# Kernel tuning notes

Hardware: AMD Instinct MI355X
Metric: run time of the kernel (lower is better)

## Reference

```python
import jax, jax.numpy as jnp
import numpy as np

B, N, K = 4, 4096, 16   # batch of graphs, nodes, kernel_size (label width)
C, T = 8, 3             # out_channels, convoTimes


def setup_inputs() -> dict:
    key = jax.random.key(0)
    k1, k2, k3 = jax.random.split(key, 3)
    labelsList = jax.random.normal(k1, (B, N, K), dtype=jnp.float32)
    # adjacency-like structure; WLC only tests >= 1, values in {0,1}
    ligand_structure = jax.random.randint(k2, (B, N, N), 0, 2, dtype=jnp.int32)
    # nn.ParameterDict of torch.rand(convoTimes, kernel_size) per channel -> [C, T, K]
    kernels = jax.random.uniform(k3, (C, T, K), dtype=jnp.float32)
    return {"labelsList": labelsList, "ligand_structure": ligand_structure, "kernels": kernels}


def reference(labelsList, ligand_structure, kernels):
    # mask[b,n,s] = 1 if ligand_structure[b][n][s] >= 1 (thresholded adjacency)
    mask = (ligand_structure >= 1).astype(labelsList.dtype)  # [B,N,N]
    # newLabelsList = labelsList.repeat(out_channels,1,1) -> [B,C,N,K]
    X0 = jnp.broadcast_to(labelsList[:, None], (B, C, N, K))
    # Each convo step reads a snapshot (cal_list) taken before the step, so:
    #   X_{t+1}[c] = X_t[c] + (mask @ X_t[c]) * kernels[c, t]
    def step(X, kt):  # kt: [C,K] = kernels[:, t, :]
        agg = jnp.einsum('bns,bcsk->bcnk', mask, X)  # masked sparse-dense matmul
        return X + agg * kt[None, :, None, :], None

    Xf, _ = jax.lax.scan(step, X0, jnp.swapaxes(kernels, 0, 1))  # scan over T steps
    return Xf  # [B,C,N,K]
```

## Files before the change

kernel.cpp:

```cpp
#include <hip/hip_runtime.h>


#define BB 4
#define NN 4096
#define KK 16
#define CC 8
#define TT 3
#define WPR (NN / 64)
#define YSWZ (KK * NN)

typedef unsigned long long u64;
typedef unsigned int u32;
typedef unsigned short u16;
typedef __attribute__((ext_vector_type(8))) short s16x8;
typedef __attribute__((ext_vector_type(4))) float f32x4v;

__device__ __forceinline__ u32 bf16_rne(float f) {
    u32 u = __float_as_uint(f);
    return (u + 0x7FFFu + ((u >> 16) & 1u)) >> 16;
}
__device__ __forceinline__ float bf16_f32(u32 h) {
    return __uint_as_float(h << 16);
}
__device__ __forceinline__ long ypos(int f, int s) {
    return ((long)(s >> 8) << 12) + (s & 3) * 1024 + ((s >> 7) & 1) * 512 +
           f * 32 + ((s >> 5) & 3) * 8 + ((s >> 2) & 7);
}

__device__ __forceinline__ s16x8 expand8(u32 byt) {
    u32 n0 = byt & 0xFu, n1 = (byt >> 4) & 0xFu;
    u32 t0 = (n0 * 0x204081u) & 0x01010101u;
    u32 t1 = (n1 * 0x204081u) & 0x01010101u;
    u32 m0 = (t0 << 7) - t0;
    u32 m1 = (t1 << 7) - t1;
    union { u32 w[4]; s16x8 v; } u;
    u.w[0] = __builtin_amdgcn_perm(0u, m0, 0x0C010C00u) << 7;
    u.w[1] = __builtin_amdgcn_perm(0u, m0, 0x0C030C02u) << 7;
    u.w[2] = __builtin_amdgcn_perm(0u, m1, 0x0C010C00u) << 7;
    u.w[3] = __builtin_amdgcn_perm(0u, m1, 0x0C030C02u) << 7;
    return u.v;
}

__global__ __launch_bounds__(256)
void prep_kernel(const float* __restrict__ labels, u16* __restrict__ ysw0) {
    int gid = blockIdx.x * 256 + threadIdx.x;
    int s4 = (gid & (NN / 4 - 1)) * 4;
    int f  = (gid >> 10) & (KK - 1);
    int b  = gid >> 14;
    long base = (long)b * YSWZ + ypos(f, s4);
    const float* lp = labels + ((long)b * NN + s4) * KK + f;
#pragma unroll
    for (int j = 0; j < 4; ++j)
        ysw0[base + j * 1024] = (u16)bf16_rne(lp[j * KK]);
}

__global__ __launch_bounds__(256, 4)
void spmm1_k(const int* __restrict__ lig, u64* __restrict__ bits,
             const u16* __restrict__ yin, u16* __restrict__ yout)
{
    __shared__ float red[3][4][64];
    __shared__ u64 bl[64][16];
    const int bid = blockIdx.x;
    const int rt  = bid & (NN / 16 - 1);
    const int b   = bid >> 8;
    const int tid = threadIdx.x;
    const int lane = tid & 63, ss = tid >> 6;
    const int n16 = lane & 15, g = lane >> 4;
    const int row0 = rt * 16;

    const u16* yb = yin + (long)b * YSWZ + (ss * 16) * 1024 + n16 * 32 + g * 8;
    s16x8 p0[4], p1[4];
#pragma unroll
    for (int i = 0; i < 4; ++i) {
        p0[i] = *(const s16x8*)(yb + i * 1024);
        p1[i] = *(const s16x8*)(yb + i * 1024 + 512);
    }

    {
        const int* lrow = lig + ((long)b * NN + row0) * NN;
        auto laddr = [&](int i) {
            int row = (ss * 4) + (i >> 4), w4 = i & 15;
            return (const int4*)(lrow + (long)row * NN + w4 * 256 + lane * 4);
        };
        int4 v[4];
#pragma unroll
        for (int i = 0; i < 4; ++i) v[i] = *laddr(i);
#pragma unroll 4
        for (int i = 0; i < 64; ++i) {
            const int slot = i & 3;
            int4 cur = v[slot];
            if (i + 4 < 64) v[slot] = *laddr(i + 4);
            u64 m0 = __ballot(cur.x >= 1);
            u64 m1 = __ballot(cur.y >= 1);
            u64 m2 = __ballot(cur.z >= 1);
            u64 m3 = __ballot(cur.w >= 1);
            if (lane == 0) {
                int row = (ss * 4) + (i >> 4), wq = (i & 15) * 4;
                bl[wq + 0][row] = m0; bl[wq + 1][row] = m1;
                bl[wq + 2][row] = m2; bl[wq + 3][row] = m3;
            }
        }
        __syncthreads();
        uint4* dst = (uint4*)(bits + (long)(b * (NN / 16) + rt) * 1024);
        const uint4* src = (const uint4*)&bl[0][0];
        dst[tid]       = src[tid];
        dst[tid + 256] = src[tid + 256];
    }

    u64 wcs[16];
#pragma unroll
    for (int wi = 0; wi < 16; ++wi) wcs[wi] = bl[ss * 16 + wi][n16];

    f32x4v accA = {0.f, 0.f, 0.f, 0.f}, accB = {0.f, 0.f, 0.f, 0.f};
#pragma unroll
    for (int wi = 0; wi < 16; ++wi) {
        const int slot = wi & 3;
        s16x8 b0 = p0[slot], b1 = p1[slot];
        if (wi + 4 < 16) {
            p0[slot] = *(const s16x8*)(yb + (wi + 4) * 1024);
            p1[slot] = *(const s16x8*)(yb + (wi + 4) * 1024 + 512);
        }
        u64 h = wcs[wi] >> (g * 8);
        accA = __builtin_amdgcn_mfma_f32_16x16x32_bf16(expand8((u32)h & 0xFFu), b0, accA, 0, 0, 0);
        accB = __builtin_amdgcn_mfma_f32_16x16x32_bf16(expand8(((u32)(h >> 32)) & 0xFFu), b1, accB, 0, 0, 0);
    }

    f32x4v acc;
#pragma unroll
    for (int r = 0; r < 4; ++r) acc[r] = accA[r] + accB[r];

    if (ss != 0) {
#pragma unroll
        for (int r = 0; r < 4; ++r) red[ss - 1][r][lane] = acc[r];
    }
    __syncthreads();
    if (ss == 0) {
#pragma unroll
        for (int r = 0; r < 4; ++r)
            acc[r] += red[0][r][lane] + red[1][r][lane] + red[2][r][lane];
        const int s0 = row0 + 4 * g;
        const long ybase = (long)b * YSWZ + ypos(n16, s0);
#pragma unroll
        for (int r = 0; r < 4; ++r)
            yout[ybase + r * 1024] = (u16)bf16_rne(acc[r]);
    }
}

template<bool LAST>
__global__ __launch_bounds__(256, 2)
void spmm2_k(const u64* __restrict__ bits, const u16* __restrict__ yin,
             u16* __restrict__ yout, const u16* __restrict__ ysw1,
             const u16* __restrict__ ysw2, const float* __restrict__ labels,
             const float* __restrict__ ker, float* __restrict__ out)
{
    __shared__ float red[2][3][4][64];
    __shared__ float t1[32][16], t2[32][16], t3[32][16];
    const int bid = blockIdx.x;
    const int rtp = bid & (NN / 32 - 1);
    const int b   = bid >> 7;
    const int tid = threadIdx.x;
    const int lane = tid & 63, ss = tid >> 6;
    const int n16 = lane & 15, g = lane >> 4;
    const int row0 = rtp * 32;
    const int rt0 = 2 * rtp, rt1 = 2 * rtp + 1;

    const u64* bb0 = bits + ((long)(b * (NN / 16) + rt0) * 64 + ss * 16) * 16 + n16;
    const u64* bb1 = bits + ((long)(b * (NN / 16) + rt1) * 64 + ss * 16) * 16 + n16;
    const u16* yb  = yin + (long)b * YSWZ + (ss * 16) * 1024 + n16 * 32 + g * 8;

    s16x8 p0[4], p1[4]; u64 m0[4], m1[4];
#pragma unroll
    for (int i = 0; i < 4; ++i) {
        p0[i] = *(const s16x8*)(yb + i * 1024);
        p1[i] = *(const s16x8*)(yb + i * 1024 + 512);
        m0[i] = bb0[i * 16];
        m1[i] = bb1[i * 16];
    }

    f32x4v accA0 = {0.f,0.f,0.f,0.f}, accB0 = {0.f,0.f,0.f,0.f};
    f32x4v accA1 = {0.f,0.f,0.f,0.f}, accB1 = {0.f,0.f,0.f,0.f};
#pragma unroll
    for (int wi = 0; wi < 16; ++wi) {
        const int slot = wi & 3;
        s16x8 b0 = p0[slot], b1 = p1[slot];
        u64 h0 = m0[slot], h1 = m1[slot];
        if (wi + 4 < 16) {
            p0[slot] = *(const s16x8*)(yb + (wi + 4) * 1024);
            p1[slot] = *(const s16x8*)(yb + (wi + 4) * 1024 + 512);
            m0[slot] = bb0[(wi + 4) * 16];
            m1[slot] = bb1[(wi + 4) * 16];
        }
        u64 ha = h0 >> (g * 8), hb = h1 >> (g * 8);
        accA0 = __builtin_amdgcn_mfma_f32_16x16x32_bf16(expand8((u32)ha & 0xFFu), b0, accA0, 0, 0, 0);
        accB0 = __builtin_amdgcn_mfma_f32_16x16x32_bf16(expand8(((u32)(ha >> 32)) & 0xFFu), b1, accB0, 0, 0, 0);
        accA1 = __builtin_amdgcn_mfma_f32_16x16x32_bf16(expand8((u32)hb & 0xFFu), b0, accA1, 0, 0, 0);
        accB1 = __builtin_amdgcn_mfma_f32_16x16x32_bf16(expand8(((u32)(hb >> 32)) & 0xFFu), b1, accB1, 0, 0, 0);
    }

    f32x4v acc0, acc1;
#pragma unroll
    for (int r = 0; r < 4; ++r) { acc0[r] = accA0[r] + accB0[r];
                                  acc1[r] = accA1[r] + accB1[r]; }

    const int s0a = row0 + 4 * g;
    const int s0b = row0 + 16 + 4 * g;
    const long yba = (long)b * YSWZ + ypos(n16, s0a);
    const long ybb = (long)b * YSWZ + ypos(n16, s0b);
    float y1a[4], y2a[4], y1b[4], y2b[4];
    if (LAST && ss == 0) {
#pragma unroll
        for (int r = 0; r < 4; ++r) {
            y1a[r] = bf16_f32(ysw1[yba + r * 1024]);
            y2a[r] = bf16_f32(ysw2[yba + r * 1024]);
            y1b[r] = bf16_f32(ysw1[ybb + r * 1024]);
            y2b[r] = bf16_f32(ysw2[ybb + r * 1024]);
        }
    }

    if (ss != 0) {
#pragma unroll
        for (int r = 0; r < 4; ++r) {
            red[0][ss - 1][r][lane] = acc0[r];
            red[1][ss - 1][r][lane] = acc1[r];
        }
    }
    __syncthreads();
    if (ss == 0) {
#pragma unroll
        for (int r = 0; r < 4; ++r) {
            acc0[r] += red[0][0][r][lane] + red[0][1][r][lane] + red[0][2][r][lane];
            acc1[r] += red[1][0][r][lane] + red[1][1][r][lane] + red[1][2][r][lane];
        }
        if (!LAST) {
#pragma unroll
            for (int r = 0; r < 4; ++r) {
                yout[yba + r * 1024] = (u16)bf16_rne(acc0[r]);
                yout[ybb + r * 1024] = (u16)bf16_rne(acc1[r]);
            }
        } else {
#pragma unroll
            for (int r = 0; r < 4; ++r) {
                t1[4 * g + r][n16]      = y1a[r];
                t2[4 * g + r][n16]      = y2a[r];
                t3[4 * g + r][n16]      = acc0[r];
                t1[16 + 4 * g + r][n16] = y1b[r];
                t2[16 + 4 * g + r][n16] = y2b[r];
                t3[16 + 4 * g + r][n16] = acc1[r];
            }
        }
    }

    if (LAST) {
        __syncthreads();
#pragma unroll
        for (int j = 0; j < 4; ++j) {
            int fi = tid + j * 256;
            int c = fi >> 7, row = (fi >> 2) & 31, k4 = fi & 3;
            const float4* kf = (const float4*)ker;
            float4 a = kf[(c * TT + 0) * 4 + k4];
            float4 d = kf[(c * TT + 1) * 4 + k4];
            float4 e = kf[(c * TT + 2) * 4 + k4];
            float4 e1, e2, e3;
            e1.x = a.x + d.x + e.x;               e1.y = a.y + d.y + e.y;
            e1.z = a.z + d.z + e.z;               e1.w = a.w + d.w + e.w;
            e2.x = a.x*d.x + a.x*e.x + d.x*e.x;   e2.y = a.y*d.y + a.y*e.y + d.y*e.y;
            e2.z = a.z*d.z + a.z*e.z + d.z*e.z;   e2.w = a.w*d.w + a.w*e.w + d.w*e.w;
            e3.x = a.x * d.x * e.x;               e3.y = a.y * d.y * e.y;
            e3.z = a.z * d.z * e.z;               e3.w = a.w * d.w * e.w;
            float4 y0 = *(const float4*)(labels + ((long)b * NN + row0 + row) * KK + k4 * 4);
            float4 v1 = *(const float4*)&t1[row][k4 * 4];
            float4 v2 = *(const float4*)&t2[row][k4 * 4];
            float4 v3 = *(const float4*)&t3[row][k4 * 4];
            float4 r;
            r.x = y0.x + e1.x * v1.x + e2.x * v2.x + e3.x * v3.x;
            r.y = y0.y + e1.y * v1.y + e2.y * v2.y + e3.y * v3.y;
            r.z = y0.z + e1.z * v1.z + e2.z * v2.z + e3.z * v3.z;
            r.w = y0.w + e1.w * v1.w + e2.w * v2.w + e3.w * v3.w;
            *(float4*)(out + (((long)b * CC + c) * NN + row0 + row) * KK + k4 * 4) = r;
        }
    }
}

extern "C" void kernel_launch(void* const* d_in, const int* in_sizes, int n_in,
                              void* d_out, int out_size, void* d_ws, size_t ws_size,
                              hipStream_t stream) {
    const float* labels = (const float*)d_in[0];
    const int*   lig    = (const int*)d_in[1];
    const float* ker    = (const float*)d_in[2];
    float* out = (float*)d_out;

    u64* bits = (u64*)d_ws;
    u16* ysw0 = (u16*)((char*)d_ws + (long)BB * WPR * NN * 8);
    u16* ysw1 = ysw0 + (long)BB * YSWZ;
    u16* ysw2 = ysw1 + (long)BB * YSWZ;

    hipLaunchKernelGGL(prep_kernel, dim3(256), dim3(256), 0, stream,
                       labels, ysw0);

    hipLaunchKernelGGL(spmm1_k, dim3(BB * (NN / 16)), dim3(256), 0, stream,
                       lig, bits, ysw0, ysw1);
    hipLaunchKernelGGL((spmm2_k<false>), dim3(BB * (NN / 32)), dim3(256), 0,
                       stream, bits, ysw1, ysw2, (const u16*)nullptr,
                       (const u16*)nullptr, (const float*)nullptr,
                       (const float*)nullptr, (float*)nullptr);
    hipLaunchKernelGGL((spmm2_k<true>),  dim3(BB * (NN / 32)), dim3(256), 0,
                       stream, bits, ysw2, (u16*)nullptr, ysw1, ysw2,
                       labels, ker, out);
}
```

Before: 81.54 us.

## Reassign mask columns per wave so each wave's MFMA runs without a block barrier

Each wave now reads the adjacency tile for its own column range across all 16 rows instead of 4 full rows. That way the bitmask words a wave needs for its MFMA slice are produced by that same wave, so the barrier between mask packing and the matmul is removed and the two are interleaved per group of four words. The adjacency reads also switch to nontemporal loads, and the global write of the packed bits moves after the reduction barrier. A risk: intra-wave LDS visibility relies on the lane-0 writes being ordered before the other lanes' reads without an explicit wave barrier, and the row access pattern is less sequential.

```diff
diff --git a/kernel.cpp b/kernel.cpp
--- a/kernel.cpp
+++ b/kernel.cpp
@@ -14,6 +14,7 @@
 typedef unsigned short u16;
 typedef __attribute__((ext_vector_type(8))) short s16x8;
 typedef __attribute__((ext_vector_type(4))) float f32x4v;
+typedef __attribute__((ext_vector_type(4))) int i32x4;
 
 __device__ __forceinline__ u32 bf16_rne(float f) {
     u32 u = __float_as_uint(f);
@@ -76,64 +77,67 @@
         p1[i] = *(const s16x8*)(yb + i * 1024 + 512);
     }
 
+    const int* lrow = lig + ((long)b * NN + row0) * NN;
+    auto laddr = [&](int i) {
+        int row = i & 15, w4 = ss * 4 + (i >> 4);
+        return (const i32x4*)(lrow + (long)row * NN + w4 * 256 + lane * 4);
+    };
+    i32x4 v[4];
+#pragma unroll
+    for (int i = 0; i < 4; ++i) v[i] = __builtin_nontemporal_load(laddr(i));
+
+    f32x4v accA = {0.f, 0.f, 0.f, 0.f}, accB = {0.f, 0.f, 0.f, 0.f};
+
+#pragma unroll
+    for (int j = 0; j < 4; ++j) {
+#pragma unroll 4
+        for (int t = 0; t < 16; ++t) {
+            const int i = j * 16 + t;
+            const int slot = i & 3;
+            i32x4 cur = v[slot];
+            if (i + 4 < 64) v[slot] = __builtin_nontemporal_load(laddr(i + 4));
+            u64 m0 = __ballot(cur[0] >= 1);
+            u64 m1 = __ballot(cur[1] >= 1);
+            u64 m2 = __ballot(cur[2] >= 1);
+            u64 m3 = __ballot(cur[3] >= 1);
+            if (lane == 0) {
+                const int wq = (ss * 4 + j) * 4;
+                bl[wq + 0][t] = m0; bl[wq + 1][t] = m1;
+                bl[wq + 2][t] = m2; bl[wq + 3][t] = m3;
+            }
+        }
+#pragma unroll
+        for (int k = 0; k < 4; ++k) {
+            const int wi = 4 * j + k;
+            const int slot = wi & 3;
+            u64 h = bl[ss * 16 + wi][n16] >> (g * 8);
+            s16x8 b0 = p0[slot], b1 = p1[slot];
+            if (wi + 4 < 16) {
+                p0[slot] = *(const s16x8*)(yb + (wi + 4) * 1024);
+                p1[slot] = *(const s16x8*)(yb + (wi + 4) * 1024 + 512);
+            }
+            accA = __builtin_amdgcn_mfma_f32_16x16x32_bf16(expand8((u32)h & 0xFFu), b0, accA, 0, 0, 0);
+            accB = __builtin_amdgcn_mfma_f32_16x16x32_bf16(expand8(((u32)(h >> 32)) & 0xFFu), b1, accB, 0, 0, 0);
+        }
+    }
+
+    f32x4v acc;
+#pragma unroll
+    for (int r = 0; r < 4; ++r) acc[r] = accA[r] + accB[r];
+
+    if (ss != 0) {
+#pragma unroll
+        for (int r = 0; r < 4; ++r) red[ss - 1][r][lane] = acc[r];
+    }
+    __syncthreads();
+
     {
-        const int* lrow = lig + ((long)b * NN + row0) * NN;
-        auto laddr = [&](int i) {
-            int row = (ss * 4) + (i >> 4), w4 = i & 15;
-            return (const int4*)(lrow + (long)row * NN + w4 * 256 + lane * 4);
-        };
-        int4 v[4];
-#pragma unroll
-        for (int i = 0; i < 4; ++i) v[i] = *laddr(i);
-#pragma unroll 4
-        for (int i = 0; i < 64; ++i) {
-            const int slot = i & 3;
-            int4 cur = v[slot];
-            if (i + 4 < 64) v[slot] = *laddr(i + 4);
-            u64 m0 = __ballot(cur.x >= 1);
-            u64 m1 = __ballot(cur.y >= 1);
-            u64 m2 = __ballot(cur.z >= 1);
-            u64 m3 = __ballot(cur.w >= 1);
-            if (lane == 0) {
-                int row = (ss * 4) + (i >> 4), wq = (i & 15) * 4;
-                bl[wq + 0][row] = m0; bl[wq + 1][row] = m1;
-                bl[wq + 2][row] = m2; bl[wq + 3][row] = m3;
-            }
-        }
-        __syncthreads();
         uint4* dst = (uint4*)(bits + (long)(b * (NN / 16) + rt) * 1024);
         const uint4* src = (const uint4*)&bl[0][0];
         dst[tid]       = src[tid];
         dst[tid + 256] = src[tid + 256];
     }
 
-    u64 wcs[16];
-#pragma unroll
-    for (int wi = 0; wi < 16; ++wi) wcs[wi] = bl[ss * 16 + wi][n16];
-
-    f32x4v accA = {0.f, 0.f, 0.f, 0.f}, accB = {0.f, 0.f, 0.f, 0.f};
-#pragma unroll
-    for (int wi = 0; wi < 16; ++wi) {
-        const int slot = wi & 3;
-        s16x8 b0 = p0[slot], b1 = p1[slot];
-        if (wi + 4 < 16) {
-            p0[slot] = *(const s16x8*)(yb + (wi + 4) * 1024);
-            p1[slot] = *(const s16x8*)(yb + (wi + 4) * 1024 + 512);
-        }
-        u64 h = wcs[wi] >> (g * 8);
-        accA = __builtin_amdgcn_mfma_f32_16x16x32_bf16(expand8((u32)h & 0xFFu), b0, accA, 0, 0, 0);
-        accB = __builtin_amdgcn_mfma_f32_16x16x32_bf16(expand8(((u32)(h >> 32)) & 0xFFu), b1, accB, 0, 0, 0);
-    }
-
-    f32x4v acc;
-#pragma unroll
-    for (int r = 0; r < 4; ++r) acc[r] = accA[r] + accB[r];
-
-    if (ss != 0) {
-#pragma unroll
-        for (int r = 0; r < 4; ++r) red[ss - 1][r][lane] = acc[r];
-    }
-    __syncthreads();
     if (ss == 0) {
 #pragma unroll
         for (int r = 0; r < 4; ++r)
```

Result: slower. 83.94 us (+2.9%).

## Split adjacency bit-packing from first SpMM and fold prep into pack kernel

Applied to the files above, without the earlier changes.

Replaces the fused pack+first-SpMM kernel with a dedicated pack kernel that only thresholds the adjacency into bitmasks, using twice as many blocks (each handling half a row tile) with a deeper load pipeline. The bf16 label conversion formerly done in a separate prep launch is folded into the same kernel. The first propagation step now runs through the bits-based spmm2 kernel like the others. This removes one launch and aims for better memory-bandwidth utilisation on the large int32 adjacency read, at the cost of an extra SpMM kernel launch that re-reads the packed bits.

```diff
diff --git a/kernel.cpp b/kernel.cpp
--- a/kernel.cpp
+++ b/kernel.cpp
@@ -41,109 +41,58 @@
     return u.v;
 }
 
-__global__ __launch_bounds__(256)
-void prep_kernel(const float* __restrict__ labels, u16* __restrict__ ysw0) {
-    int gid = blockIdx.x * 256 + threadIdx.x;
-    int s4 = (gid & (NN / 4 - 1)) * 4;
-    int f  = (gid >> 10) & (KK - 1);
-    int b  = gid >> 14;
-    long base = (long)b * YSWZ + ypos(f, s4);
-    const float* lp = labels + ((long)b * NN + s4) * KK + f;
-#pragma unroll
-    for (int j = 0; j < 4; ++j)
-        ysw0[base + j * 1024] = (u16)bf16_rne(lp[j * KK]);
-}
-
 __global__ __launch_bounds__(256, 4)
-void spmm1_k(const int* __restrict__ lig, u64* __restrict__ bits,
-             const u16* __restrict__ yin, u16* __restrict__ yout)
+void pack_kernel(const int* __restrict__ lig, u64* __restrict__ bits,
+                 const float* __restrict__ labels, u16* __restrict__ ysw0)
 {
-    __shared__ float red[3][4][64];
-    __shared__ u64 bl[64][16];
+    __shared__ u64 bl[32][16];
     const int bid = blockIdx.x;
-    const int rt  = bid & (NN / 16 - 1);
-    const int b   = bid >> 8;
+    const int h   = bid & 1;
+    const int rt  = (bid >> 1) & 255;
+    const int b   = bid >> 9;
     const int tid = threadIdx.x;
     const int lane = tid & 63, ss = tid >> 6;
-    const int n16 = lane & 15, g = lane >> 4;
     const int row0 = rt * 16;
 
-    const u16* yb = yin + (long)b * YSWZ + (ss * 16) * 1024 + n16 * 32 + g * 8;
-    s16x8 p0[4], p1[4];
-#pragma unroll
-    for (int i = 0; i < 4; ++i) {
-        p0[i] = *(const s16x8*)(yb + i * 1024);
-        p1[i] = *(const s16x8*)(yb + i * 1024 + 512);
-    }
-
-    {
-        const int* lrow = lig + ((long)b * NN + row0) * NN;
-        auto laddr = [&](int i) {
-            int row = (ss * 4) + (i >> 4), w4 = i & 15;
-            return (const int4*)(lrow + (long)row * NN + w4 * 256 + lane * 4);
-        };
-        int4 v[4];
-#pragma unroll
-        for (int i = 0; i < 4; ++i) v[i] = *laddr(i);
+    int gid = bid * 256 + tid;
+    if (gid < BB * KK * (NN / 4)) {
+        int s4 = (gid & (NN / 4 - 1)) * 4;
+        int f  = (gid >> 10) & (KK - 1);
+        int pb = gid >> 14;
+        long base = (long)pb * YSWZ + ypos(f, s4);
+        const float* lp = labels + ((long)pb * NN + s4) * KK + f;
+#pragma unroll
+        for (int j = 0; j < 4; ++j)
+            ysw0[base + j * 1024] = (u16)bf16_rne(lp[j * KK]);
+    }
+
+    const int* lrow = lig + ((long)b * NN + row0) * NN + h * 2048;
+    auto laddr = [&](int i) {
+        int row = i & 15, w4l = ss * 2 + (i >> 4);
+        return (const int4*)(lrow + (long)row * NN + w4l * 256 + lane * 4);
+    };
+    int4 v[8];
+#pragma unroll
+    for (int i = 0; i < 8; ++i) v[i] = *laddr(i);
 #pragma unroll 4
-        for (int i = 0; i < 64; ++i) {
-            const int slot = i & 3;
-            int4 cur = v[slot];
-            if (i + 4 < 64) v[slot] = *laddr(i + 4);
-            u64 m0 = __ballot(cur.x >= 1);
-            u64 m1 = __ballot(cur.y >= 1);
-            u64 m2 = __ballot(cur.z >= 1);
-            u64 m3 = __ballot(cur.w >= 1);
-            if (lane == 0) {
-                int row = (ss * 4) + (i >> 4), wq = (i & 15) * 4;
-                bl[wq + 0][row] = m0; bl[wq + 1][row] = m1;
-                bl[wq + 2][row] = m2; bl[wq + 3][row] = m3;
-            }
-        }
-        __syncthreads();
-        uint4* dst = (uint4*)(bits + (long)(b * (NN / 16) + rt) * 1024);
-        const uint4* src = (const uint4*)&bl[0][0];
-        dst[tid]       = src[tid];
-        dst[tid + 256] = src[tid + 256];
-    }
-
-    u64 wcs[16];
-#pragma unroll
-    for (int wi = 0; wi < 16; ++wi) wcs[wi] = bl[ss * 16 + wi][n16];
-
-    f32x4v accA = {0.f, 0.f, 0.f, 0.f}, accB = {0.f, 0.f, 0.f, 0.f};
-#pragma unroll
-    for (int wi = 0; wi < 16; ++wi) {
-        const int slot = wi & 3;
-        s16x8 b0 = p0[slot], b1 = p1[slot];
-        if (wi + 4 < 16) {
-            p0[slot] = *(const s16x8*)(yb + (wi + 4) * 1024);
-            p1[slot] = *(const s16x8*)(yb + (wi + 4) * 1024 + 512);
-        }
-        u64 h = wcs[wi] >> (g * 8);
-        accA = __builtin_amdgcn_mfma_f32_16x16x32_bf16(expand8((u32)h & 0xFFu), b0, accA, 0, 0, 0);
-        accB = __builtin_amdgcn_mfma_f32_16x16x32_bf16(expand8(((u32)(h >> 32)) & 0xFFu), b1, accB, 0, 0, 0);
-    }
-
-    f32x4v acc;
-#pragma unroll
-    for (int r = 0; r < 4; ++r) acc[r] = accA[r] + accB[r];
-
-    if (ss != 0) {
-#pragma unroll
-        for (int r = 0; r < 4; ++r) red[ss - 1][r][lane] = acc[r];
+    for (int i = 0; i < 32; ++i) {
+        const int slot = i & 7;
+        int4 cur = v[slot];
+        if (i + 8 < 32) v[slot] = *laddr(i + 8);
+        u64 m0 = __ballot(cur.x >= 1);
+        u64 m1 = __ballot(cur.y >= 1);
+        u64 m2 = __ballot(cur.z >= 1);
+        u64 m3 = __ballot(cur.w >= 1);
+        if (lane == 0) {
+            const int row = i & 15;
+            const int wql = (ss * 2 + (i >> 4)) * 4;
+            bl[wql + 0][row] = m0; bl[wql + 1][row] = m1;
+            bl[wql + 2][row] = m2; bl[wql + 3][row] = m3;
+        }
     }
     __syncthreads();
-    if (ss == 0) {
-#pragma unroll
-        for (int r = 0; r < 4; ++r)
-            acc[r] += red[0][r][lane] + red[1][r][lane] + red[2][r][lane];
-        const int s0 = row0 + 4 * g;
-        const long ybase = (long)b * YSWZ + ypos(n16, s0);
-#pragma unroll
-        for (int r = 0; r < 4; ++r)
-            yout[ybase + r * 1024] = (u16)bf16_rne(acc[r]);
-    }
+    uint4* dst = (uint4*)(bits + (long)(b * 256 + rt) * 1024 + h * 512);
+    dst[tid] = ((const uint4*)&bl[0][0])[tid];
 }
 
 template<bool LAST>
@@ -294,16 +243,19 @@
     u16* ysw1 = ysw0 + (long)BB * YSWZ;
     u16* ysw2 = ysw1 + (long)BB * YSWZ;
 
-    hipLaunchKernelGGL(prep_kernel, dim3(256), dim3(256), 0, stream,
-                       labels, ysw0);
-
-    hipLaunchKernelGGL(spmm1_k, dim3(BB * (NN / 16)), dim3(256), 0, stream,
-                       lig, bits, ysw0, ysw1);
-    hipLaunchKernelGGL((spmm2_k<false>), dim3(BB * (NN / 32)), dim3(256), 0,
-                       stream, bits, ysw1, ysw2, (const u16*)nullptr,
+    hipLaunchKernelGGL(pack_kernel, dim3(BB * 256 * 2), dim3(256), 0, stream,
+                       lig, bits, labels, ysw0);
+
+    dim3 sgrid(BB * (NN / 32));
+    hipLaunchKernelGGL((spmm2_k<false>), sgrid, dim3(256), 0, stream,
+                       bits, ysw0, ysw1, (const u16*)nullptr,
                        (const u16*)nullptr, (const float*)nullptr,
                        (const float*)nullptr, (float*)nullptr);
-    hipLaunchKernelGGL((spmm2_k<true>),  dim3(BB * (NN / 32)), dim3(256), 0,
-                       stream, bits, ysw2, (u16*)nullptr, ysw1, ysw2,
+    hipLaunchKernelGGL((spmm2_k<false>), sgrid, dim3(256), 0, stream,
+                       bits, ysw1, ysw2, (const u16*)nullptr,
+                       (const u16*)nullptr, (const float*)nullptr,
+                       (const float*)nullptr, (float*)nullptr);
+    hipLaunchKernelGGL((spmm2_k<true>),  sgrid, dim3(256), 0, stream,
+                       bits, ysw2, (u16*)nullptr, ysw1, ysw2,
                        labels, ker, out);
 }
```

Result: slower. 163.5 us (+100.6%).
